# Optimization experiments

Hardware: AMD Instinct MI355X
Metric: run time of the kernel (lower is better)

## Reference

```python
import jax, jax.numpy as jnp
import numpy as np

N_NODES = 25000
N_EDGES = 400000
N_GRAPHS = 100
D_IN = 16
D = 32          # node_dim
K = 11          # spectral coefficients = edge_dim
NOUT1 = 30
NOUT2 = 2
L = 2           # n_interactions
D_OUT = 32


def setup_inputs() -> dict:
    key = jax.random.key(0)
    ks = jax.random.split(key, 24)
    s = 0.1
    inp = {
        'x': jax.random.normal(ks[0], (N_NODES, D_IN), jnp.float32),
        'edge_attr': jax.random.uniform(ks[1], (N_EDGES, K), jnp.float32),
        'edge_index': jax.random.randint(ks[2], (2, N_EDGES), 0, N_NODES),
        'batch': jnp.sort(jax.random.randint(ks[3], (N_NODES,), 0, N_GRAPHS)),
        # embedding
        'emb_w': jax.random.normal(ks[4], (D_IN, D)) * s,
        'emb_b': jnp.zeros((D,)),
        # per-interaction params, stacked on leading L axis
        'init_w': jax.random.normal(ks[5], (L, D, D)) * s,             # initial_dense (no bias)
        'e1_w': jax.random.normal(ks[6], (L, K, 2 * K)) * s,
        'e2_w': jax.random.normal(ks[7], (L, K, 2 * K)) * s,
        'e3_w': jax.random.normal(ks[8], (L, K, 2 * K)) * s,
        'e4_w': jax.random.normal(ks[9], (L, 4 * K, K)) * s,
        'conv_w': jax.random.normal(ks[10], (L, K, D, NOUT1)) * s,     # SpectConv weight (selfconn=False)
        'conv_b': jnp.zeros((L, NOUT1)),
        'att_v': jax.random.normal(ks[11], (L, D, 1)) * s,
        'skip1_w': jax.random.normal(ks[12], (L, D, NOUT2)) * s,
        'skip1_b': jnp.full((L, NOUT2), 0.01),
        'skip2_w': jax.random.normal(ks[13], (L, D, NOUT2)) * s,
        'skip2_b': jnp.full((L, NOUT2), 0.01),
        'out_w': jax.random.normal(ks[14], (L, NOUT1 + NOUT2, D)) * s,
        'out_b': jnp.full((L, D), 0.01),
        # encoder output head
        'final_w': jax.random.normal(ks[15], (D, D_OUT)) * s,
        'final_b': jnp.zeros((D_OUT,)),
    }
    return inp


def _segment_softmax(raw, dst, n):
    m = jax.ops.segment_max(raw, dst, num_segments=n)
    m = jnp.where(jnp.isfinite(m), m, 0.0)
    e = jnp.exp(raw - m[dst])
    denom = jax.ops.segment_sum(e, dst, num_segments=n)
    return e / (denom[dst] + 1e-16)


def _interaction(h, src, dst, edge_attr, p):
    (init_w, e1_w, e2_w, e3_w, e4_w, conv_w, conv_b, att_v,
     s1_w, s1_b, s2_w, s2_b, out_w, out_b) = p
    n = h.shape[0]
    h_proj = h @ init_w                                     # [N, D]
    # learned edge transform
    lin = jax.nn.relu(edge_attr @ e1_w)                     # [E, 2K]
    gate = jnp.tanh(edge_attr @ e2_w) * jnp.tanh(edge_attr @ e3_w)
    ea = jax.nn.relu(jnp.concatenate([lin, gate], axis=1) @ e4_w)  # [E, K]
    # spectral conv with attention (selfconn=False)
    xs = h_proj[src]                                        # gather [E, D]
    msgs = ea[:, :, None] * xs[:, None, :]                  # [E, K, D]
    agg = jax.ops.segment_sum(msgs, dst, num_segments=n)    # [N, K, D]
    sum_out = jnp.einsum('nkd,kdo->no', agg, conv_w)        # [N, NOUT1]
    pooled = ea.mean(axis=1, keepdims=True) * xs            # mean_k msg_k, [E, D]
    raw_att = (pooled @ att_v)[:, 0]                        # [E]
    att = _segment_softmax(raw_att, dst, n)                 # [E]
    att_agg = jax.ops.segment_sum(att[:, None, None] * msgs, dst, num_segments=n)
    att_out = jnp.einsum('nkd,kdo->no', att_agg, conv_w)
    conv_out = jax.nn.relu(sum_out + att_out + conv_b)      # [N, NOUT1]
    skip = jnp.tanh(h_proj @ s1_w + s1_b) * jnp.tanh(h_proj @ s2_w + s2_b)  # [N, NOUT2]
    layer_out = jnp.concatenate([conv_out, skip], axis=1)
    delta = layer_out @ out_w + out_b                       # [N, D]
    return delta, att


def reference(x, edge_attr, emb_w, emb_b, init_w, e1_w, e2_w, e3_w, e4_w,
              conv_w, conv_b, att_v, skip1_w, skip1_b, skip2_w, skip2_b,
              out_w, out_b, final_w, final_b, edge_index, batch):
    src, dst = edge_index[0], edge_index[1]
    h = x @ emb_w + emb_b                                   # node embedding [N, D]
    atts = []
    for l in range(L):
        p = (init_w[l], e1_w[l], e2_w[l], e3_w[l], e4_w[l], conv_w[l], conv_b[l],
             att_v[l], skip1_w[l], skip1_b[l], skip2_w[l], skip2_b[l], out_w[l], out_b[l])
        delta, att = _interaction(h, src, dst, edge_attr, p)
        h = h + delta                                       # residual
        atts.append(att)
    # global mean pool per graph
    counts = jax.ops.segment_sum(jnp.ones((h.shape[0],), h.dtype), batch, num_segments=N_GRAPHS)
    pooled = jax.ops.segment_sum(h, batch, num_segments=N_GRAPHS) / jnp.maximum(counts, 1.0)[:, None]
    output = pooled @ final_w + final_b                     # [G, D_OUT]
    return output, h, jnp.stack(atts)
```

## Files before the change

kernel.cpp:

```cpp
#include <hip/hip_runtime.h>
#include <hip/hip_bf16.h>

typedef __hip_bfloat16 bf16;
using f32x4v = __attribute__((ext_vector_type(4))) float;
using bf16x8 = __attribute__((ext_vector_type(8))) short;

#define N_NODES 25000
#define N_PAD   25024
#define N_EDGES 400000
#define N_GR    100

__device__ __forceinline__ bf16 tob(float v) { return __float2bfloat16(v); }
__device__ __forceinline__ unsigned short tobu(float v) {
  union { bf16 b; unsigned short u; } c; c.b = __float2bfloat16(v); return c.u;
}
__device__ __forceinline__ float b2f(unsigned short u) { return __uint_as_float(((unsigned)u) << 16); }
__device__ __forceinline__ float tanh_fast(float x) {
  float cx = fminf(fmaxf(x, -10.f), 10.f);
  float e = __expf(2.f * cx);
  return (e - 1.f) / (e + 1.f);
}

__global__ __launch_bounds__(256) void hist_kernel(const int* __restrict__ dst, int* __restrict__ deg, int E) {
  int e = blockIdx.x * blockDim.x + threadIdx.x;
  if (e < E) atomicAdd(&deg[dst[e]], 1);
}

__global__ __launch_bounds__(1024) void scan_kernel(const int* __restrict__ deg, int* __restrict__ offs,
                                                    int* __restrict__ cur, int n) {
  __shared__ int wsum[16];
  __shared__ int wpre[16];
  int t = threadIdx.x, lane = t & 63, w = t >> 6;
  int carry = 0;
  for (int base = 0; base < n; base += 1024) {
    int v = (base + t < n) ? deg[base + t] : 0;
    int x = v;
    #pragma unroll
    for (int s = 1; s < 64; s <<= 1) { int y = __shfl_up(x, s); if (lane >= s) x += y; }
    if (lane == 63) wsum[w] = x;
    __syncthreads();
    if (w == 0 && lane < 16) {
      int ws_ = wsum[lane];
      int xs = ws_;
      #pragma unroll
      for (int s = 1; s < 16; s <<= 1) { int y = __shfl_up(xs, s); if (lane >= s) xs += y; }
      wpre[lane] = xs - ws_;
    }
    __syncthreads();
    int excl = carry + wpre[w] + x - v;
    if (base + t < n) { offs[base + t] = excl; cur[base + t] = excl; }
    carry += wpre[15] + wsum[15];
    __syncthreads();
  }
  if (t == 0) offs[n] = carry;
}

__global__ __launch_bounds__(256) void fill_kernel(const int* __restrict__ dst, int* __restrict__ cur,
                                                   int* __restrict__ elist, int E) {
  int e = blockIdx.x * blockDim.x + threadIdx.x;
  if (e < E) { int p = atomicAdd(&cur[dst[e]], 1); elist[p] = e; }
}

__global__ __launch_bounds__(256) void prep_kernel(const float* __restrict__ e1, const float* __restrict__ e2,
                                                   const float* __restrict__ e3, const float* __restrict__ e4,
                                                   const float* __restrict__ attv, const float* __restrict__ convw,
                                                   const float* __restrict__ outw,
                                                   float* __restrict__ wE, bf16* __restrict__ Wt,
                                                   bf16* __restrict__ owB) {
  int i = blockIdx.x * blockDim.x + threadIdx.x;
  if (i < 2 * 1352) {
    int l = i / 1352, r = i % 1352;
    float v = 0.f;
    if (r < 264)       { int q = r;        int j = q / 12, k = q % 12; if (k < 11) v = e1[l*242 + k*22 + j]; }
    else if (r < 528)  { int q = r - 264;  int j = q / 12, k = q % 12; if (k < 11) v = e2[l*242 + k*22 + j]; }
    else if (r < 792)  { int q = r - 528;  int j = q / 12, k = q % 12; if (k < 11) v = e3[l*242 + k*22 + j]; }
    else if (r < 1056) { int q = r - 792;  int j = q / 12, k = q % 12; if (k < 11) v = e4[l*484 + j*11 + k]; }
    else if (r < 1320) { int q = r - 1056; int j = q / 12, k = q % 12; if (k < 11) v = e4[l*484 + (22 + j)*11 + k]; }
    else               { int d = r - 1320; v = attv[l*32 + d]; }
    wE[i] = v;
  }
  int t = i - 2 * 1352;
  if (t >= 0 && t < 2 * 32 * 352) {
    int l = t / (32 * 352), q = t % (32 * 352);
    int o = q / 352, dk = q % 352;
    int d = dk / 11, kk = dk % 11;
    float v = 0.f;
    if (o < 30) v = convw[l*10560 + (kk*32 + d)*30 + o];
    Wt[t] = tob(v);
  }
  int u = i - 2 * 1352 - 2 * 32 * 352;
  if (u >= 0 && u < 2048) {
    int l = u >> 10, rem = u & 1023;
    int hf = rem >> 9, rem2 = rem & 511;
    int lane = rem2 >> 3, j = rem2 & 7;
    int k = (lane >> 4) * 8 + j, n = lane & 15;
    owB[u] = tob(outw[l*1024 + k*32 + hf*16 + n]);
  }
}

__global__ __launch_bounds__(256) void emb_kernel(const float* __restrict__ x, const float* __restrict__ w,
                                                  const float* __restrict__ b, float* __restrict__ h, int N) {
  __shared__ float sw[16 * 32];
  __shared__ float sb[32];
  for (int i = threadIdx.x; i < 16 * 32; i += blockDim.x) sw[i] = w[i];
  if (threadIdx.x < 32) sb[threadIdx.x] = b[threadIdx.x];
  __syncthreads();
  int i = blockIdx.x * blockDim.x + threadIdx.x;
  if (i >= N * 32) return;
  int n = i >> 5, d = i & 31;
  float acc = sb[d];
  #pragma unroll
  for (int k = 0; k < 16; k++) acc += x[n*16 + k] * sw[k*32 + d];
  h[i] = acc;
}

__global__ __launch_bounds__(256) void hproj_kernel(const float* __restrict__ h, const float* __restrict__ w,
                                                    float* __restrict__ hp, unsigned short* __restrict__ hpb, int N) {
  __shared__ float sw[32 * 32];
  for (int i = threadIdx.x; i < 32 * 32; i += blockDim.x) sw[i] = w[i];
  __syncthreads();
  int i = blockIdx.x * blockDim.x + threadIdx.x;
  if (i >= N * 32) return;
  int n = i >> 5, d = i & 31;
  const float* hr = h + (size_t)n * 32;
  float acc = 0.f;
  #pragma unroll
  for (int k = 0; k < 32; k++) acc += hr[k] * sw[k*32 + d];
  hp[i] = acc;
  hpb[i] = tobu(acc);
}

__device__ __forceinline__ void loadw12(const float4* base, int idx3, float* w) {
  float4 a = base[idx3], b = base[idx3 + 1], c = base[idx3 + 2];
  w[0]=a.x; w[1]=a.y; w[2]=a.z; w[3]=a.w;
  w[4]=b.x; w[5]=b.y; w[6]=b.z; w[7]=b.w;
  w[8]=c.x; w[9]=c.y; w[10]=c.z; w[11]=c.w;
}

__global__ __launch_bounds__(256) void edge_kernel(const float* __restrict__ eattr,
                                                   const int* __restrict__ srcA,
                                                   const unsigned short* __restrict__ hpb,
                                                   const float* __restrict__ wEl,
                                                   uint2* __restrict__ eab, float* __restrict__ raw_out, int E) {
  const float4* w4 = (const float4*)wEl;
  int e = blockIdx.x * blockDim.x + threadIdx.x;
  bool live = e < E;
  float a[11], acc[11];
  #pragma unroll
  for (int k = 0; k < 11; k++) {
    a[k] = live ? eattr[(size_t)e*11 + k] : 0.f;
    acc[k] = 0.f;
  }
  for (int j = 0; j < 22; j++) {
    float w[12];
    loadw12(w4, j*3, w);
    float l1 = 0.f;
    #pragma unroll
    for (int k = 0; k < 11; k++) l1 += a[k] * w[k];
    loadw12(w4, 66 + j*3, w);
    float l2 = 0.f;
    #pragma unroll
    for (int k = 0; k < 11; k++) l2 += a[k] * w[k];
    loadw12(w4, 132 + j*3, w);
    float l3 = 0.f;
    #pragma unroll
    for (int k = 0; k < 11; k++) l3 += a[k] * w[k];
    float gg = tanh_fast(l2) * tanh_fast(l3);
    l1 = fmaxf(l1, 0.f);
    float wl[12], wg[12];
    loadw12(w4, 198 + j*3, wl);
    loadw12(w4, 264 + j*3, wg);
    #pragma unroll
    for (int k = 0; k < 11; k++) acc[k] += l1*wl[k] + gg*wg[k];
  }
  if (!live) return;
  const float* av = wEl + 1320;
  float mean = 0.f;
  #pragma unroll
  for (int k = 0; k < 11; k++) { acc[k] = fmaxf(acc[k], 0.f); mean += acc[k]; }
  mean *= (1.f / 11.f);
  unsigned p[6];
  #pragma unroll
  for (int q = 0; q < 5; q++)
    p[q] = (unsigned)tobu(acc[2*q]) | ((unsigned)tobu(acc[2*q+1]) << 16);
  p[5] = (unsigned)tobu(acc[10]);
  uint2* er = eab + (size_t)e * 3;
  er[0] = make_uint2(p[0], p[1]);
  er[1] = make_uint2(p[2], p[3]);
  er[2] = make_uint2(p[4], p[5]);
  int s = srcA[e];
  const uint2* hb = (const uint2*)(hpb + (size_t)s * 32);
  float dot = 0.f;
  #pragma unroll
  for (int q = 0; q < 8; q++) {
    uint2 hv = hb[q];
    dot += b2f((unsigned short)hv.x) * av[q*4+0] + b2f((unsigned short)(hv.x >> 16)) * av[q*4+1]
         + b2f((unsigned short)hv.y) * av[q*4+2] + b2f((unsigned short)(hv.y >> 16)) * av[q*4+3];
  }
  raw_out[e] = mean * dot;
}

__device__ __forceinline__ void unpack_ev(uint2 q0, uint2 q1, uint2 q2, float* ev) {
  ev[0] = b2f((unsigned short)q0.x); ev[1] = b2f((unsigned short)(q0.x >> 16));
  ev[2] = b2f((unsigned short)q0.y); ev[3] = b2f((unsigned short)(q0.y >> 16));
  ev[4] = b2f((unsigned short)q1.x); ev[5] = b2f((unsigned short)(q1.x >> 16));
  ev[6] = b2f((unsigned short)q1.y); ev[7] = b2f((unsigned short)(q1.y >> 16));
  ev[8] = b2f((unsigned short)q2.x); ev[9] = b2f((unsigned short)(q2.x >> 16));
  ev[10] = b2f((unsigned short)q2.y);
}

__global__ __launch_bounds__(256) void node_kernel(const int* __restrict__ offs, const int* __restrict__ elist,
                                                   const int* __restrict__ srcA,
                                                   const uint2* __restrict__ eab, const float* __restrict__ raw,
                                                   const unsigned short* __restrict__ hpb,
                                                   bf16* __restrict__ Abuf, float* __restrict__ atts, int N) {
  int wid = threadIdx.x >> 6, lane = threadIdx.x & 63;
  int half = lane >> 5, d = lane & 31;
  int n = blockIdx.x * 4 + wid;
  if (n >= N_PAD) return;
  bool valid = (n < N);
  int beg = 0, deg = 0;
  if (valid) { beg = offs[n]; deg = offs[n + 1] - beg; }

  float agg[11], watt[11];
  #pragma unroll
  for (int k = 0; k < 11; k++) { agg[k] = 0.f; watt[k] = 0.f; }
  float m = -1e30f, denom = 0.f;

  int j = half;
  for (; j + 2 < deg; j += 4) {
    int ia = elist[beg + j], ib = elist[beg + j + 2];
    int sa = srcA[ia], sb = srcA[ib];
    float xa = b2f(hpb[(size_t)sa * 32 + d]);
    float xb = b2f(hpb[(size_t)sb * 32 + d]);
    float ra = raw[ia], rb = raw[ib];
    uint2 a0 = eab[(size_t)ia * 3], a1 = eab[(size_t)ia * 3 + 1], a2 = eab[(size_t)ia * 3 + 2];
    uint2 b0 = eab[(size_t)ib * 3], b1 = eab[(size_t)ib * 3 + 1], b2q = eab[(size_t)ib * 3 + 2];
    float eva[11], evb[11];
    unpack_ev(a0, a1, a2, eva);
    unpack_ev(b0, b1, b2q, evb);
    if (ra > m) {
      float sc = __expf(m - ra);
      denom *= sc;
      #pragma unroll
      for (int k = 0; k < 11; k++) watt[k] *= sc;
      m = ra;
    }
    float pa = __expf(ra - m);
    denom += pa;
    #pragma unroll
    for (int k = 0; k < 11; k++) { float t = eva[k]; agg[k] += t * xa; watt[k] += (pa * t) * xa; }
    if (rb > m) {
      float sc = __expf(m - rb);
      denom *= sc;
      #pragma unroll
      for (int k = 0; k < 11; k++) watt[k] *= sc;
      m = rb;
    }
    float pb = __expf(rb - m);
    denom += pb;
    #pragma unroll
    for (int k = 0; k < 11; k++) { float t = evb[k]; agg[k] += t * xb; watt[k] += (pb * t) * xb; }
  }
  for (; j < deg; j += 2) {
    int eid = elist[beg + j];
    int s = srcA[eid];
    float xs = b2f(hpb[(size_t)s * 32 + d]);
    float r = raw[eid];
    uint2 q0 = eab[(size_t)eid * 3], q1 = eab[(size_t)eid * 3 + 1], q2 = eab[(size_t)eid * 3 + 2];
    float ev[11];
    unpack_ev(q0, q1, q2, ev);
    if (r > m) {
      float sc = __expf(m - r);
      denom *= sc;
      #pragma unroll
      for (int k = 0; k < 11; k++) watt[k] *= sc;
      m = r;
    }
    float p = __expf(r - m);
    denom += p;
    #pragma unroll
    for (int k = 0; k < 11; k++) { float t = ev[k]; agg[k] += t * xs; watt[k] += (p * t) * xs; }
  }

  float m_o = __shfl_xor(m, 32);
  float M = fmaxf(m, m_o);
  float ss = __expf(m - M);
  float so = __expf(m_o - M);
  float den_o = __shfl_xor(denom, 32);
  float denT = denom * ss + den_o * so;
  float inv = 1.f / (denT + 1e-16f);
  float comb[11];
  #pragma unroll
  for (int k = 0; k < 11; k++) {
    float ao = __shfl_xor(agg[k], 32);
    float wo = __shfl_xor(watt[k], 32);
    comb[k] = (agg[k] + ao) + (watt[k] * ss + wo * so) * inv;
  }

  if (half == 0) {
    bf16* arow = Abuf + (size_t)n * 352 + d * 11;
    #pragma unroll
    for (int k = 0; k < 11; k++) arow[k] = tob(comb[k]);
  }

  for (int jj = lane; jj < deg; jj += 64) {
    int eid = elist[beg + jj];
    atts[eid] = __expf(raw[eid] - M) * inv;
  }
}

__global__ __launch_bounds__(256) void convfused_kernel(const short* __restrict__ A, const short* __restrict__ Wt,
                                                        const short* __restrict__ owB,
                                                        const float* __restrict__ hp, float* __restrict__ h,
                                                        const float* __restrict__ convb,
                                                        const float* __restrict__ s1w, const float* __restrict__ s1b,
                                                        const float* __restrict__ s2w, const float* __restrict__ s2b,
                                                        const float* __restrict__ outb, int N) {
  __shared__ short slo[64][40];
  __shared__ float sdelta[64][36];
  __shared__ float sskipw[128];
  __shared__ float sskipb[4];
  __shared__ float scb[32];
  __shared__ float sob[32];
  int tid = threadIdx.x;
  if (tid < 64) sskipw[tid] = s1w[tid];
  if (tid >= 64 && tid < 128) sskipw[tid] = s2w[tid - 64];
  if (tid >= 128 && tid < 160) sob[tid - 128] = outb[tid - 128];
  if (tid >= 160 && tid < 192) scb[tid - 160] = (tid - 160 < 30) ? convb[tid - 160] : 0.f;
  if (tid >= 192 && tid < 196) sskipb[tid - 192] = (tid < 194) ? s1b[tid - 192] : s2b[tid - 194];
  __syncthreads();

  int wave = tid >> 6, lane = tid & 63;
  int r16 = lane & 15, kq = lane >> 4;
  int mbase = blockIdx.x * 64 + wave * 16;

  const short* arow = A + (size_t)(mbase + r16) * 352 + kq * 8;
  const short* b0p = Wt + (size_t)r16 * 352 + kq * 8;
  const short* b1p = b0p + 16 * 352;
  f32x4v acc0 = {0.f, 0.f, 0.f, 0.f}, acc1 = {0.f, 0.f, 0.f, 0.f};
  #pragma unroll
  for (int ks = 0; ks < 11; ks++) {
    bf16x8 af = *(const bf16x8*)(arow + ks * 32);
    bf16x8 b0 = *(const bf16x8*)(b0p + ks * 32);
    bf16x8 b1 = *(const bf16x8*)(b1p + ks * 32);
    acc0 = __builtin_amdgcn_mfma_f32_16x16x32_bf16(af, b0, acc0, 0, 0, 0);
    acc1 = __builtin_amdgcn_mfma_f32_16x16x32_bf16(af, b1, acc1, 0, 0, 0);
  }
  #pragma unroll
  for (int r = 0; r < 4; r++) {
    int row = wave * 16 + kq * 4 + r;
    slo[row][r16] = (short)tobu(fmaxf(acc0[r] + scb[r16], 0.f));
    if (r16 < 14) slo[row][16 + r16] = (short)tobu(fmaxf(acc1[r] + scb[16 + r16], 0.f));
  }
  __syncthreads();

  if (tid < 128) {
    int row = tid >> 1, jx = tid & 1;
    int grow = blockIdx.x * 64 + row;
    float a1 = sskipb[jx], a2 = sskipb[2 + jx];
    if (grow < N) {
      const float* hr = hp + (size_t)grow * 32;
      #pragma unroll
      for (int dd = 0; dd < 32; dd++) {
        float hv = hr[dd];
        a1 += hv * sskipw[dd*2 + jx];
        a2 += hv * sskipw[64 + dd*2 + jx];
      }
    }
    slo[row][30 + jx] = (short)tobu(tanh_fast(a1) * tanh_fast(a2));
  }
  __syncthreads();

  bf16x8 a2f = *(const bf16x8*)&slo[wave * 16 + r16][kq * 8];
  bf16x8 bo0 = *(const bf16x8*)(owB + lane * 8);
  bf16x8 bo1 = *(const bf16x8*)(owB + 512 + lane * 8);
  f32x4v d0 = {0.f, 0.f, 0.f, 0.f}, d1 = {0.f, 0.f, 0.f, 0.f};
  d0 = __builtin_amdgcn_mfma_f32_16x16x32_bf16(a2f, bo0, d0, 0, 0, 0);
  d1 = __builtin_amdgcn_mfma_f32_16x16x32_bf16(a2f, bo1, d1, 0, 0, 0);
  #pragma unroll
  for (int r = 0; r < 4; r++) {
    int row = wave * 16 + kq * 4 + r;
    sdelta[row][r16] = d0[r] + sob[r16];
    sdelta[row][16 + r16] = d1[r] + sob[16 + r16];
  }
  __syncthreads();

  {
    int row = tid >> 2, col0 = (tid & 3) * 8;
    int grow = blockIdx.x * 64 + row;
    if (grow < N) {
      float* hr = h + (size_t)grow * 32 + col0;
      float4 ha = *(float4*)hr;
      float4 hb = *(float4*)(hr + 4);
      float4 da = *(float4*)&sdelta[row][col0];
      float4 db = *(float4*)&sdelta[row][col0 + 4];
      ha.x += da.x; ha.y += da.y; ha.z += da.z; ha.w += da.w;
      hb.x += db.x; hb.y += db.y; hb.z += db.z; hb.w += db.w;
      *(float4*)hr = ha;
      *(float4*)(hr + 4) = hb;
    }
  }
}

__global__ void bounds_kernel(const int* __restrict__ batch, int* __restrict__ gb) {
  int g = threadIdx.x;
  if (g > N_GR) return;
  if (g == N_GR) { gb[g] = N_NODES; return; }
  int lo = 0, hi = N_NODES;
  while (lo < hi) { int mid = (lo + hi) >> 1; if (batch[mid] < g) lo = mid + 1; else hi = mid; }
  gb[g] = lo;
}

__global__ __launch_bounds__(256) void pool2_kernel(const float* __restrict__ h, const int* __restrict__ gb,
                                                    const float* __restrict__ fw, const float* __restrict__ fb,
                                                    float* __restrict__ out0, float* __restrict__ outh) {
  __shared__ float part[8][32];
  __shared__ float pooled[32];
  int g = blockIdx.x;
  int s = gb[g], e = gb[g + 1];
  int grp = threadIdx.x >> 5, d = threadIdx.x & 31;
  float acc = 0.f;
  for (int n = s + grp; n < e; n += 8) {
    float v = h[(size_t)n * 32 + d];
    outh[(size_t)n * 32 + d] = v;
    acc += v;
  }
  part[grp][d] = acc;
  __syncthreads();
  if (threadIdx.x < 32) {
    float sum = 0.f;
    #pragma unroll
    for (int i = 0; i < 8; i++) sum += part[i][d];
    pooled[d] = sum / fmaxf((float)(e - s), 1.f);
  }
  __syncthreads();
  if (threadIdx.x < 32) {
    int jx = threadIdx.x;
    float o = fb[jx];
    #pragma unroll
    for (int dd = 0; dd < 32; dd++) o += pooled[dd] * fw[dd*32 + jx];
    out0[g * 32 + jx] = o;
  }
}

extern "C" void kernel_launch(void* const* d_in, const int* in_sizes, int n_in,
                              void* d_out, int out_size, void* d_ws, size_t ws_size,
                              hipStream_t stream) {
  (void)in_sizes; (void)n_in; (void)out_size; (void)ws_size;
  const float* x      = (const float*)d_in[0];
  const float* eattr  = (const float*)d_in[1];
  const int* eidx     = (const int*)d_in[2];
  const int* batch    = (const int*)d_in[3];
  const float* emb_w  = (const float*)d_in[4];
  const float* emb_b  = (const float*)d_in[5];
  const float* init_w = (const float*)d_in[6];
  const float* e1w    = (const float*)d_in[7];
  const float* e2w    = (const float*)d_in[8];
  const float* e3w    = (const float*)d_in[9];
  const float* e4w    = (const float*)d_in[10];
  const float* convw  = (const float*)d_in[11];
  const float* convb  = (const float*)d_in[12];
  const float* attv   = (const float*)d_in[13];
  const float* s1w    = (const float*)d_in[14];
  const float* s1b    = (const float*)d_in[15];
  const float* s2w    = (const float*)d_in[16];
  const float* s2b    = (const float*)d_in[17];
  const float* outw   = (const float*)d_in[18];
  const float* outb   = (const float*)d_in[19];
  const float* finw   = (const float*)d_in[20];
  const float* finb   = (const float*)d_in[21];

  char* ws = (char*)d_ws;
  size_t off = 0;
  auto take = [&](size_t bytes) -> char* {
    char* p = ws + off;
    off += (bytes + 255) & ~(size_t)255;
    return p;
  };
  float* h    = (float*)take((size_t)N_NODES * 32 * 4);
  float* hp   = (float*)take((size_t)N_NODES * 32 * 4);
  unsigned short* hpb = (unsigned short*)take((size_t)N_NODES * 32 * 2);
  uint2* eab  = (uint2*)take((size_t)N_EDGES * 24);
  float* raw  = (float*)take((size_t)N_EDGES * 4);
  bf16*  Abuf = (bf16*)take((size_t)N_PAD * 352 * 2);
  int*   deg  = (int*)take((size_t)N_NODES * 4);
  int*   offs = (int*)take((size_t)(N_NODES + 1) * 4);
  int*   cur  = (int*)take((size_t)N_NODES * 4);
  int*   elist= (int*)take((size_t)N_EDGES * 4);
  int*   gb   = (int*)take((size_t)(N_GR + 1) * 4);
  float* wE   = (float*)take((size_t)2 * 1352 * 4);
  bf16*  Wt   = (bf16*)take((size_t)2 * 32 * 352 * 2);
  bf16*  owB  = (bf16*)take((size_t)2048 * 2);

  float* out0 = (float*)d_out;
  float* outh = out0 + N_GR * 32;
  float* outa = outh + (size_t)N_NODES * 32;

  const int* srcA = eidx;
  const int* dstA = eidx + N_EDGES;

  hipMemsetAsync(deg, 0, (size_t)N_NODES * 4, stream);

  prep_kernel<<<107, 256, 0, stream>>>(e1w, e2w, e3w, e4w, attv, convw, outw, wE, Wt, owB);
  hist_kernel<<<(N_EDGES + 255) / 256, 256, 0, stream>>>(dstA, deg, N_EDGES);
  scan_kernel<<<1, 1024, 0, stream>>>(deg, offs, cur, N_NODES);
  fill_kernel<<<(N_EDGES + 255) / 256, 256, 0, stream>>>(dstA, cur, elist, N_EDGES);
  emb_kernel<<<(N_NODES * 32 + 255) / 256, 256, 0, stream>>>(x, emb_w, emb_b, h, N_NODES);
  bounds_kernel<<<1, 128, 0, stream>>>(batch, gb);

  for (int l = 0; l < 2; l++) {
    hproj_kernel<<<(N_NODES * 32 + 255) / 256, 256, 0, stream>>>(h, init_w + l * 1024, hp, hpb, N_NODES);
    edge_kernel<<<(N_EDGES + 255) / 256, 256, 0, stream>>>(
        eattr, srcA, hpb, wE + l * 1352, eab, raw, N_EDGES);
    node_kernel<<<N_PAD / 4, 256, 0, stream>>>(offs, elist, srcA, eab, raw, hpb,
                                               Abuf, outa + (size_t)l * N_EDGES, N_NODES);
    convfused_kernel<<<N_PAD / 64, 256, 0, stream>>>(
        (const short*)Abuf, (const short*)Wt + (size_t)l * 32 * 352, (const short*)owB + (size_t)l * 1024,
        hp, h, convb + l * 30, s1w + l * 64, s1b + l * 2, s2w + l * 64, s2b + l * 2,
        outb + l * 32, N_NODES);
  }

  pool2_kernel<<<N_GR, 256, 0, stream>>>(h, gb, finw, finb, out0, outh);
}
```

Measured before the change: 277.3 us.

## Scatter edge payload into dst-sorted order and fuse hproj into neighbor kernels

```diff
diff --git a/kernel.cpp b/kernel.cpp
--- a/kernel.cpp
+++ b/kernel.cpp
@@ -56,9 +56,9 @@
 }
 
 __global__ __launch_bounds__(256) void fill_kernel(const int* __restrict__ dst, int* __restrict__ cur,
-                                                   int* __restrict__ elist, int E) {
+                                                   int* __restrict__ elist, int* __restrict__ epos, int E) {
   int e = blockIdx.x * blockDim.x + threadIdx.x;
-  if (e < E) { int p = atomicAdd(&cur[dst[e]], 1); elist[p] = e; }
+  if (e < E) { int p = atomicAdd(&cur[dst[e]], 1); elist[p] = e; epos[e] = p; }
 }
 
 __global__ __launch_bounds__(256) void prep_kernel(const float* __restrict__ e1, const float* __restrict__ e2,
@@ -98,36 +98,40 @@
   }
 }
 
-__global__ __launch_bounds__(256) void emb_kernel(const float* __restrict__ x, const float* __restrict__ w,
-                                                  const float* __restrict__ b, float* __restrict__ h, int N) {
-  __shared__ float sw[16 * 32];
+__global__ __launch_bounds__(256) void emb_hproj_kernel(const float* __restrict__ x, const float* __restrict__ w,
+                                                        const float* __restrict__ b, const float* __restrict__ w1,
+                                                        float* __restrict__ h, float* __restrict__ hp,
+                                                        unsigned short* __restrict__ hpb, int N) {
+  __shared__ float semb[16 * 32];
+  __shared__ float sw1[32 * 32];
   __shared__ float sb[32];
-  for (int i = threadIdx.x; i < 16 * 32; i += blockDim.x) sw[i] = w[i];
-  if (threadIdx.x < 32) sb[threadIdx.x] = b[threadIdx.x];
-  __syncthreads();
-  int i = blockIdx.x * blockDim.x + threadIdx.x;
-  if (i >= N * 32) return;
-  int n = i >> 5, d = i & 31;
+  __shared__ float sx[8][16];
+  __shared__ float sh[8][33];
+  int tid = threadIdx.x;
+  for (int i = tid; i < 16 * 32; i += 256) semb[i] = w[i];
+  for (int i = tid; i < 32 * 32; i += 256) sw1[i] = w1[i];
+  if (tid < 32) sb[tid] = b[tid];
+  int nb = blockIdx.x * 8;
+  if (tid < 128) {
+    int n = nb + (tid >> 4), k = tid & 15;
+    sx[tid >> 4][k] = (n < N) ? x[(size_t)n * 16 + k] : 0.f;
+  }
+  __syncthreads();
+  int grp = tid >> 5, d = tid & 31;
+  int n = nb + grp;
   float acc = sb[d];
   #pragma unroll
-  for (int k = 0; k < 16; k++) acc += x[n*16 + k] * sw[k*32 + d];
-  h[i] = acc;
-}
-
-__global__ __launch_bounds__(256) void hproj_kernel(const float* __restrict__ h, const float* __restrict__ w,
-                                                    float* __restrict__ hp, unsigned short* __restrict__ hpb, int N) {
-  __shared__ float sw[32 * 32];
-  for (int i = threadIdx.x; i < 32 * 32; i += blockDim.x) sw[i] = w[i];
-  __syncthreads();
-  int i = blockIdx.x * blockDim.x + threadIdx.x;
-  if (i >= N * 32) return;
-  int n = i >> 5, d = i & 31;
-  const float* hr = h + (size_t)n * 32;
-  float acc = 0.f;
-  #pragma unroll
-  for (int k = 0; k < 32; k++) acc += hr[k] * sw[k*32 + d];
-  hp[i] = acc;
-  hpb[i] = tobu(acc);
+  for (int k = 0; k < 16; k++) acc += sx[grp][k] * semb[k*32 + d];
+  sh[grp][d] = acc;
+  if (n < N) h[(size_t)n * 32 + d] = acc;
+  __syncthreads();
+  float hpv = 0.f;
+  #pragma unroll
+  for (int k = 0; k < 32; k++) hpv += sh[grp][k] * sw1[k*32 + d];
+  if (n < N) {
+    hp[(size_t)n * 32 + d] = hpv;
+    hpb[(size_t)n * 32 + d] = tobu(hpv);
+  }
 }
 
 __device__ __forceinline__ void loadw12(const float4* base, int idx3, float* w) {
@@ -139,9 +143,10 @@
 
 __global__ __launch_bounds__(256) void edge_kernel(const float* __restrict__ eattr,
                                                    const int* __restrict__ srcA,
+                                                   const int* __restrict__ epos,
                                                    const unsigned short* __restrict__ hpb,
                                                    const float* __restrict__ wEl,
-                                                   uint2* __restrict__ eab, float* __restrict__ raw_out, int E) {
+                                                   uint4* __restrict__ pay, int E) {
   const float4* w4 = (const float4*)wEl;
   int e = blockIdx.x * blockDim.x + threadIdx.x;
   bool live = e < E;
@@ -179,15 +184,6 @@
   #pragma unroll
   for (int k = 0; k < 11; k++) { acc[k] = fmaxf(acc[k], 0.f); mean += acc[k]; }
   mean *= (1.f / 11.f);
-  unsigned p[6];
-  #pragma unroll
-  for (int q = 0; q < 5; q++)
-    p[q] = (unsigned)tobu(acc[2*q]) | ((unsigned)tobu(acc[2*q+1]) << 16);
-  p[5] = (unsigned)tobu(acc[10]);
-  uint2* er = eab + (size_t)e * 3;
-  er[0] = make_uint2(p[0], p[1]);
-  er[1] = make_uint2(p[2], p[3]);
-  er[2] = make_uint2(p[4], p[5]);
   int s = srcA[e];
   const uint2* hb = (const uint2*)(hpb + (size_t)s * 32);
   float dot = 0.f;
@@ -197,21 +193,28 @@
     dot += b2f((unsigned short)hv.x) * av[q*4+0] + b2f((unsigned short)(hv.x >> 16)) * av[q*4+1]
          + b2f((unsigned short)hv.y) * av[q*4+2] + b2f((unsigned short)(hv.y >> 16)) * av[q*4+3];
   }
-  raw_out[e] = mean * dot;
-}
-
-__device__ __forceinline__ void unpack_ev(uint2 q0, uint2 q1, uint2 q2, float* ev) {
-  ev[0] = b2f((unsigned short)q0.x); ev[1] = b2f((unsigned short)(q0.x >> 16));
-  ev[2] = b2f((unsigned short)q0.y); ev[3] = b2f((unsigned short)(q0.y >> 16));
-  ev[4] = b2f((unsigned short)q1.x); ev[5] = b2f((unsigned short)(q1.x >> 16));
-  ev[6] = b2f((unsigned short)q1.y); ev[7] = b2f((unsigned short)(q1.y >> 16));
-  ev[8] = b2f((unsigned short)q2.x); ev[9] = b2f((unsigned short)(q2.x >> 16));
-  ev[10] = b2f((unsigned short)q2.y);
+  float raw = mean * dot;
+  unsigned p[6];
+  #pragma unroll
+  for (int q = 0; q < 5; q++)
+    p[q] = (unsigned)tobu(acc[2*q]) | ((unsigned)tobu(acc[2*q+1]) << 16);
+  p[5] = (unsigned)tobu(acc[10]);
+  int pp = epos[e];
+  pay[(size_t)pp * 2]     = make_uint4(p[0], p[1], p[2], p[3]);
+  pay[(size_t)pp * 2 + 1] = make_uint4(p[4], p[5], __float_as_uint(raw), (unsigned)s);
+}
+
+__device__ __forceinline__ void unpack_pay(uint4 p0, uint4 p1, float* ev) {
+  ev[0] = b2f((unsigned short)p0.x); ev[1] = b2f((unsigned short)(p0.x >> 16));
+  ev[2] = b2f((unsigned short)p0.y); ev[3] = b2f((unsigned short)(p0.y >> 16));
+  ev[4] = b2f((unsigned short)p0.z); ev[5] = b2f((unsigned short)(p0.z >> 16));
+  ev[6] = b2f((unsigned short)p0.w); ev[7] = b2f((unsigned short)(p0.w >> 16));
+  ev[8] = b2f((unsigned short)p1.x); ev[9] = b2f((unsigned short)(p1.x >> 16));
+  ev[10] = b2f((unsigned short)p1.y);
 }
 
 __global__ __launch_bounds__(256) void node_kernel(const int* __restrict__ offs, const int* __restrict__ elist,
-                                                   const int* __restrict__ srcA,
-                                                   const uint2* __restrict__ eab, const float* __restrict__ raw,
+                                                   const uint4* __restrict__ pay,
                                                    const unsigned short* __restrict__ hpb,
                                                    bf16* __restrict__ Abuf, float* __restrict__ atts, int N) {
   int wid = threadIdx.x >> 6, lane = threadIdx.x & 63;
@@ -229,16 +232,14 @@
 
   int j = half;
   for (; j + 2 < deg; j += 4) {
-    int ia = elist[beg + j], ib = elist[beg + j + 2];
-    int sa = srcA[ia], sb = srcA[ib];
-    float xa = b2f(hpb[(size_t)sa * 32 + d]);
-    float xb = b2f(hpb[(size_t)sb * 32 + d]);
-    float ra = raw[ia], rb = raw[ib];
-    uint2 a0 = eab[(size_t)ia * 3], a1 = eab[(size_t)ia * 3 + 1], a2 = eab[(size_t)ia * 3 + 2];
-    uint2 b0 = eab[(size_t)ib * 3], b1 = eab[(size_t)ib * 3 + 1], b2q = eab[(size_t)ib * 3 + 2];
+    uint4 a0 = pay[(size_t)(beg + j) * 2],     a1 = pay[(size_t)(beg + j) * 2 + 1];
+    uint4 b0 = pay[(size_t)(beg + j + 2) * 2], b1 = pay[(size_t)(beg + j + 2) * 2 + 1];
+    float xa = b2f(hpb[(size_t)(int)a1.w * 32 + d]);
+    float xb = b2f(hpb[(size_t)(int)b1.w * 32 + d]);
+    float ra = __uint_as_float(a1.z), rb = __uint_as_float(b1.z);
     float eva[11], evb[11];
-    unpack_ev(a0, a1, a2, eva);
-    unpack_ev(b0, b1, b2q, evb);
+    unpack_pay(a0, a1, eva);
+    unpack_pay(b0, b1, evb);
     if (ra > m) {
       float sc = __expf(m - ra);
       denom *= sc;
@@ -263,13 +264,11 @@
     for (int k = 0; k < 11; k++) { float t = evb[k]; agg[k] += t * xb; watt[k] += (pb * t) * xb; }
   }
   for (; j < deg; j += 2) {
-    int eid = elist[beg + j];
-    int s = srcA[eid];
-    float xs = b2f(hpb[(size_t)s * 32 + d]);
-    float r = raw[eid];
-    uint2 q0 = eab[(size_t)eid * 3], q1 = eab[(size_t)eid * 3 + 1], q2 = eab[(size_t)eid * 3 + 2];
+    uint4 q0 = pay[(size_t)(beg + j) * 2], q1 = pay[(size_t)(beg + j) * 2 + 1];
+    float xs = b2f(hpb[(size_t)(int)q1.w * 32 + d]);
+    float r = __uint_as_float(q1.z);
     float ev[11];
-    unpack_ev(q0, q1, q2, ev);
+    unpack_pay(q0, q1, ev);
     if (r > m) {
       float sc = __expf(m - r);
       denom *= sc;
@@ -305,8 +304,8 @@
   }
 
   for (int jj = lane; jj < deg; jj += 64) {
-    int eid = elist[beg + jj];
-    atts[eid] = __expf(raw[eid] - M) * inv;
+    float r = __uint_as_float(pay[(size_t)(beg + jj) * 2 + 1].z);
+    atts[elist[beg + jj]] = __expf(r - M) * inv;
   }
 }
 
@@ -316,19 +315,26 @@
                                                         const float* __restrict__ convb,
                                                         const float* __restrict__ s1w, const float* __restrict__ s1b,
                                                         const float* __restrict__ s2w, const float* __restrict__ s2b,
-                                                        const float* __restrict__ outb, int N) {
+                                                        const float* __restrict__ outb,
+                                                        const float* __restrict__ initw_next,
+                                                        float* __restrict__ hp_out, unsigned short* __restrict__ hpb_out,
+                                                        int N) {
   __shared__ short slo[64][40];
   __shared__ float sdelta[64][36];
   __shared__ float sskipw[128];
   __shared__ float sskipb[4];
   __shared__ float scb[32];
   __shared__ float sob[32];
+  __shared__ float sw1[1024];
   int tid = threadIdx.x;
   if (tid < 64) sskipw[tid] = s1w[tid];
   if (tid >= 64 && tid < 128) sskipw[tid] = s2w[tid - 64];
   if (tid >= 128 && tid < 160) sob[tid - 128] = outb[tid - 128];
   if (tid >= 160 && tid < 192) scb[tid - 160] = (tid - 160 < 30) ? convb[tid - 160] : 0.f;
   if (tid >= 192 && tid < 196) sskipb[tid - 192] = (tid < 194) ? s1b[tid - 192] : s2b[tid - 194];
+  if (initw_next) {
+    for (int i = tid; i < 1024; i += 256) sw1[i] = initw_next[i];
+  }
   __syncthreads();
 
   int wave = tid >> 6, lane = tid & 63;
@@ -386,19 +392,37 @@
   }
   __syncthreads();
 
-  {
-    int row = tid >> 2, col0 = (tid & 3) * 8;
-    int grow = blockIdx.x * 64 + row;
+  int row = tid >> 2, col0 = (tid & 3) * 8;
+  int grow = blockIdx.x * 64 + row;
+  if (grow < N) {
+    float* hr = h + (size_t)grow * 32 + col0;
+    float4 ha = *(float4*)hr;
+    float4 hb = *(float4*)(hr + 4);
+    float4 da = *(float4*)&sdelta[row][col0];
+    float4 db = *(float4*)&sdelta[row][col0 + 4];
+    ha.x += da.x; ha.y += da.y; ha.z += da.z; ha.w += da.w;
+    hb.x += db.x; hb.y += db.y; hb.z += db.z; hb.w += db.w;
+    *(float4*)hr = ha;
+    *(float4*)(hr + 4) = hb;
+    *(float4*)&sdelta[row][col0] = ha;
+    *(float4*)&sdelta[row][col0 + 4] = hb;
+  }
+  if (initw_next) {
+    __syncthreads();
     if (grow < N) {
-      float* hr = h + (size_t)grow * 32 + col0;
-      float4 ha = *(float4*)hr;
-      float4 hb = *(float4*)(hr + 4);
-      float4 da = *(float4*)&sdelta[row][col0];
-      float4 db = *(float4*)&sdelta[row][col0 + 4];
-      ha.x += da.x; ha.y += da.y; ha.z += da.z; ha.w += da.w;
-      hb.x += db.x; hb.y += db.y; hb.z += db.z; hb.w += db.w;
-      *(float4*)hr = ha;
-      *(float4*)(hr + 4) = hb;
+      float o[8];
+      #pragma unroll
+      for (int c = 0; c < 8; c++) o[c] = 0.f;
+      #pragma unroll
+      for (int k = 0; k < 32; k++) {
+        float hv = sdelta[row][k];
+        #pragma unroll
+        for (int c = 0; c < 8; c++) o[c] += hv * sw1[k*32 + col0 + c];
+      }
+      float* hpo = hp_out + (size_t)grow * 32 + col0;
+      unsigned short* hbo = hpb_out + (size_t)grow * 32 + col0;
+      #pragma unroll
+      for (int c = 0; c < 8; c++) { hpo[c] = o[c]; hbo[c] = tobu(o[c]); }
     }
   }
 }
@@ -481,13 +505,13 @@
   float* h    = (float*)take((size_t)N_NODES * 32 * 4);
   float* hp   = (float*)take((size_t)N_NODES * 32 * 4);
   unsigned short* hpb = (unsigned short*)take((size_t)N_NODES * 32 * 2);
-  uint2* eab  = (uint2*)take((size_t)N_EDGES * 24);
-  float* raw  = (float*)take((size_t)N_EDGES * 4);
+  uint4* pay  = (uint4*)take((size_t)N_EDGES * 32);
   bf16*  Abuf = (bf16*)take((size_t)N_PAD * 352 * 2);
   int*   deg  = (int*)take((size_t)N_NODES * 4);
   int*   offs = (int*)take((size_t)(N_NODES + 1) * 4);
   int*   cur  = (int*)take((size_t)N_NODES * 4);
   int*   elist= (int*)take((size_t)N_EDGES * 4);
+  int*   epos = (int*)take((size_t)N_EDGES * 4);
   int*   gb   = (int*)take((size_t)(N_GR + 1) * 4);
   float* wE   = (float*)take((size_t)2 * 1352 * 4);
   bf16*  Wt   = (bf16*)take((size_t)2 * 32 * 352 * 2);
@@ -505,20 +529,20 @@
   prep_kernel<<<107, 256, 0, stream>>>(e1w, e2w, e3w, e4w, attv, convw, outw, wE, Wt, owB);
   hist_kernel<<<(N_EDGES + 255) / 256, 256, 0, stream>>>(dstA, deg, N_EDGES);
   scan_kernel<<<1, 1024, 0, stream>>>(deg, offs, cur, N_NODES);
-  fill_kernel<<<(N_EDGES + 255) / 256, 256, 0, stream>>>(dstA, cur, elist, N_EDGES);
-  emb_kernel<<<(N_NODES * 32 + 255) / 256, 256, 0, stream>>>(x, emb_w, emb_b, h, N_NODES);
+  fill_kernel<<<(N_EDGES + 255) / 256, 256, 0, stream>>>(dstA, cur, elist, epos, N_EDGES);
+  emb_hproj_kernel<<<(N_NODES + 7) / 8, 256, 0, stream>>>(x, emb_w, emb_b, init_w, h, hp, hpb, N_NODES);
   bounds_kernel<<<1, 128, 0, stream>>>(batch, gb);
 
   for (int l = 0; l < 2; l++) {
-    hproj_kernel<<<(N_NODES * 32 + 255) / 256, 256, 0, stream>>>(h, init_w + l * 1024, hp, hpb, N_NODES);
     edge_kernel<<<(N_EDGES + 255) / 256, 256, 0, stream>>>(
-        eattr, srcA, hpb, wE + l * 1352, eab, raw, N_EDGES);
-    node_kernel<<<N_PAD / 4, 256, 0, stream>>>(offs, elist, srcA, eab, raw, hpb,
+        eattr, srcA, epos, hpb, wE + l * 1352, pay, N_EDGES);
+    node_kernel<<<N_PAD / 4, 256, 0, stream>>>(offs, elist, pay, hpb,
                                                Abuf, outa + (size_t)l * N_EDGES, N_NODES);
     convfused_kernel<<<N_PAD / 64, 256, 0, stream>>>(
         (const short*)Abuf, (const short*)Wt + (size_t)l * 32 * 352, (const short*)owB + (size_t)l * 1024,
         hp, h, convb + l * 30, s1w + l * 64, s1b + l * 2, s2w + l * 64, s2b + l * 2,
-        outb + l * 32, N_NODES);
+        outb + l * 32,
+        (l == 0) ? (init_w + 1024) : nullptr, hp, hpb, N_NODES);
   }
 
   pool2_kernel<<<N_GR, 256, 0, stream>>>(h, gb, finw, finb, out0, outh);
```

Result: faster. 257.8 us (-7.0%).
